# Performance work log

Hardware: AMD Instinct MI355X
Metric: run time of the kernel (lower is better)

The kernel has to match this reference:

```python
import jax, jax.numpy as jnp
import numpy as np

NF, NC, LENGTH, BATCH = 64, 16, 2048, 256
WEIGHT_BI, WEIGHT_L2 = 0.01, 0.01
BETA = 2.5     # temporal soft-min/max sharpness (TemporalOperator beta=2.5)
KAPPA = 10.0   # logical soft-min/max sharpness (avm approximation)
EPSN = 1e-12


def setup_inputs() -> dict:
    key = jax.random.key(0)
    ks = jax.random.split(key, 11)
    x = jax.random.normal(ks[0], (BATCH, LENGTH, 2), dtype=jnp.float32)
    t1 = jax.random.uniform(ks[1], (NF,), minval=0.0, maxval=float(LENGTH // 2), dtype=jnp.float32)
    t2 = jax.random.uniform(ks[2], (NF,), minval=float(LENGTH // 2), maxval=float(LENGTH), dtype=jnp.float32)
    a = jax.random.uniform(ks[3], (NF,), dtype=jnp.float32)
    b = jax.random.uniform(ks[4], (NF,), dtype=jnp.float32)
    p1 = jax.random.uniform(ks[5], (NC, NF), dtype=jnp.float32)
    p2 = jax.random.uniform(ks[6], (1, NC), dtype=jnp.float32)
    tvar_temporal = jax.random.uniform(ks[7], (NF,), dtype=jnp.float32)
    tvar_logical1 = jax.random.uniform(ks[8], (NC,), dtype=jnp.float32)
    tvar_logical2 = jax.random.uniform(ks[9], (1,), dtype=jnp.float32)
    eps = jnp.full((1,), 0.1, dtype=jnp.float32)
    return dict(x=x, t1=t1, t2=t2, a=a, b=b, p1=p1, p2=p2,
                tvar_temporal=tvar_temporal, tvar_logical1=tvar_logical1,
                tvar_logical2=tvar_logical2, eps=eps)


def _ste(v, v_new):
    # torch clamps parameter .data under no_grad -> value changes, grad is identity
    return v + jax.lax.stop_gradient(v_new - v)


def _wsel(r, logw, sharp):
    # weighted soft-max (sharp>0) / soft-min (sharp<0) along last axis
    s = jax.nn.softmax(sharp * r + logw, axis=-1)
    return jnp.sum(s * r, axis=-1)


def reference(x, t1, t2, a, b, p1, p2, tvar_temporal, tvar_logical1, tvar_logical2, eps):
    # --- in-place parameter maintenance (clamp under no_grad in torch) ---
    p1 = _ste(p1, jnp.clip(p1, 0.0, 1.0))
    p2 = _ste(p2, jnp.clip(p2, 0.0, 1.0))
    tvt = _ste(tvar_temporal, jnp.clip(tvar_temporal, 0.0, 1.0))
    tvl1 = _ste(tvar_logical1, jnp.clip(tvar_logical1, 0.0, 1.0))
    tvl2 = _ste(tvar_logical2, jnp.clip(tvar_logical2, 0.0, 1.0))
    t1c = jnp.clip(t1, 0.0, LENGTH - 1.0)
    t2c = jnp.clip(t2, 0.0, LENGTH - 1.0)
    t1c = jnp.where(t1c >= t2c - 1.0, t2c - 1.0, t1c)
    t1u = _ste(t1, t1c)
    t2u = _ste(t2, t2c)

    # --- predicates (vectorized over all nf features; dim = i % 2) ---
    dims = jnp.arange(NF) % 2
    rp = a[None, None, :] * x[:, :, dims] - b[None, None, :]     # [B, T, NF]
    rp = jnp.transpose(rp, (0, 2, 1))                             # [B, NF, T]

    # --- temporal operators: smooth window [t1, t2] + soft min/max over time ---
    tg = jnp.arange(LENGTH, dtype=x.dtype)
    w = jax.nn.sigmoid(BETA * (tg[None, :] - t1u[:, None])) * \
        jax.nn.sigmoid(BETA * (t2u[:, None] - tg[None, :]))       # [NF, T]
    logw = jnp.log(w + EPSN)[None]                                # [1, NF, T]
    rmax = _wsel(rp, logw, BETA)                                  # eventually  [B, NF]
    rmin = _wsel(rp, logw, -BETA)                                 # always      [B, NF]
    r1 = tvt[None, :] * rmax + (1.0 - tvt[None, :]) * rmin        # [B, NF]

    # --- logical layer 1: weighted soft OR/AND over features, per clause ---
    logp1 = jnp.log(p1 + EPSN)[None]                              # [1, NC, NF]
    r1e = r1[:, None, :]                                          # [B, NC, NF]
    r_or = _wsel(r1e, logp1, KAPPA)
    r_and = _wsel(r1e, logp1, -KAPPA)
    r2 = tvl1[None, :] * r_or + (1.0 - tvl1[None, :]) * r_and     # [B, NC]

    # --- logical layer 2: combine clauses ---
    logp2 = jnp.log(p2[0] + EPSN)[None]                           # [1, NC]
    r_or2 = _wsel(r2, logp2, KAPPA)
    r_and2 = _wsel(r2, logp2, -KAPPA)
    r = tvl2[0] * r_or2 + (1.0 - tvl2[0]) * r_and2                # [B]

    # --- regularizers ---
    bi = WEIGHT_BI * (jnp.sum(tvt * (1.0 - tvt)) + jnp.sum(tvl1 * (1.0 - tvl1)) +
                      jnp.sum(tvl2 * (1.0 - tvl2)) + jnp.sum(p1 * (1.0 - p1)) +
                      jnp.sum(p2 * (1.0 - p2)))
    l2 = WEIGHT_L2 * (jnp.sum(p1 * p1) + jnp.sum(p2 * p2))
    reg = bi + l2
    return r, reg
```

## Files before the change

### kernel.cpp

```cpp
#include <hip/hip_runtime.h>
#include <math.h>

#define NF 64
#define NC 16
#define LEN 2048
#define BATCH 256
#define BETA 2.5f
#define KAPPA 10.0f
#define EPSN 1e-12f
#define LOG2E 1.4426950408889634f

#define TPB 1024
#define NQ (TPB / NF)
#define CHUNK (LEN / NQ)

__device__ __forceinline__ float clip01(float v) { return fminf(fmaxf(v, 0.0f), 1.0f); }

__device__ __forceinline__ float fexp2(float x) {
#if __has_builtin(__builtin_amdgcn_exp2f)
    return __builtin_amdgcn_exp2f(x);
#else
    return exp2f(x);
#endif
}

__device__ __forceinline__ float frcp(float x) {
#if __has_builtin(__builtin_amdgcn_rcpf)
    return __builtin_amdgcn_rcpf(x);
#else
    return 1.0f / x;
#endif
}

__global__ __launch_bounds__(TPB) void fused_kernel(
    const float* __restrict__ x, const float* __restrict__ t1g,
    const float* __restrict__ t2g, const float* __restrict__ av,
    const float* __restrict__ bv, const float* __restrict__ p1,
    const float* __restrict__ p2, const float* __restrict__ tvt_,
    const float* __restrict__ tvl1_, const float* __restrict__ tvl2_,
    float* __restrict__ out) {
    __shared__ float4 redQ[NQ][NF];
    __shared__ float r1s[NF];
    __shared__ float r2s[NC];

    const int b = blockIdx.x;
    const int tid = threadIdx.x;
    const int f = tid & (NF - 1);
    const int q = tid >> 6;
    const int ch = f & 1;

    const float B2 = BETA * LOG2E;
    const float KL = KAPPA * LOG2E;

    const float a = av[f];
    const float A2 = B2 * a;

    float t1c = fminf(fmaxf(t1g[f], 0.0f), (float)(LEN - 1));
    float t2c = fminf(fmaxf(t2g[f], 0.0f), (float)(LEN - 1));
    t1c = fminf(t1c, t2c - 1.0f);
    const float c1 = B2 * t1c;
    const float c2 = -B2 * t2c;

    const int t0 = q * CHUNK;
    const float4* xp4 = (const float4*)(x + (size_t)b * (LEN * 2) + 2 * t0);

    float Sp0 = 0.f, Xp0 = 0.f, Sm0 = 0.f, Xm0 = 0.f;
    float Sp1 = 0.f, Xp1 = 0.f, Sm1 = 0.f, Xm1 = 0.f;
#pragma unroll 4
    for (int k2 = 0; k2 < CHUNK / 2; ++k2) {
        float4 v = xp4[k2];
        float xa = ch ? v.y : v.x;
        float xb = ch ? v.w : v.z;
        float tfa = (float)(t0 + 2 * k2);
        float tfb = tfa + 1.0f;

        {
            float g1 = fmaf(-B2, tfa, c1);
            float g2 = fmaf(B2, tfa, c2);
            float den = (1.0f + fexp2(g1)) * (1.0f + fexp2(g2));
            float w = frcp(den);
            float P = fexp2(A2 * xa);
            float Pm = frcp(P);
            float tp = P * w, tm = Pm * w;
            Sp0 += tp; Xp0 = fmaf(tp, xa, Xp0);
            Sm0 += tm; Xm0 = fmaf(tm, xa, Xm0);
        }
        {
            float g1 = fmaf(-B2, tfb, c1);
            float g2 = fmaf(B2, tfb, c2);
            float den = (1.0f + fexp2(g1)) * (1.0f + fexp2(g2));
            float w = frcp(den);
            float P = fexp2(A2 * xb);
            float Pm = frcp(P);
            float tp = P * w, tm = Pm * w;
            Sp1 += tp; Xp1 = fmaf(tp, xb, Xp1);
            Sm1 += tm; Xm1 = fmaf(tm, xb, Xm1);
        }
    }

    redQ[q][f] = make_float4(Sp0 + Sp1, Xp0 + Xp1, Sm0 + Sm1, Xm0 + Xm1);

    if (b == 0 && q == NQ - 1) {
        const int l = f;
        float acc = 0.0f;
#pragma unroll
        for (int i = 0; i < 16; ++i) {
            float p = clip01(p1[i * NF + l]);
            acc += 0.01f * (p * (1.0f - p)) + 0.01f * (p * p);
        }
        {
            float c = clip01(tvt_[l]);
            acc += 0.01f * (c * (1.0f - c));
        }
        if (l < NC) {
            float p = clip01(p2[l]);
            acc += 0.01f * (p * (1.0f - p)) + 0.01f * (p * p);
            float c = clip01(tvl1_[l]);
            acc += 0.01f * (c * (1.0f - c));
        }
        if (l == 0) {
            float c = clip01(tvl2_[0]);
            acc += 0.01f * (c * (1.0f - c));
        }
#pragma unroll
        for (int d = 1; d < 64; d <<= 1) acc += __shfl_xor(acc, d);
        if (l == 0) out[BATCH] = acc;
    }

    __syncthreads();
    if (tid >= 64) return;

    const int l = tid;
    float ax = 0.f, ay = 0.f, az = 0.f, aw = 0.f;
#pragma unroll
    for (int s = 0; s < NQ; ++s) {
        float4 v = redQ[s][l];
        ax += v.x; ay += v.y; az += v.z; aw += v.w;
    }
    {
        float af = av[l], bf = bv[l];
        float tvt = clip01(tvt_[l]);
        float rmax = af * (ay / ax);
        float rmin = af * (aw / az);
        r1s[l] = tvt * rmax + (1.0f - tvt) * rmin - bf;
    }

    {
        const int c = l & 15;
        const int j = l >> 4;
        float so = 0.f, wo = 0.f, sa = 0.f, wa = 0.f;
#pragma unroll
        for (int i = 0; i < 16; ++i) {
            int ff = j * 16 + i;
            float r1v = r1s[ff];
            float lg = __log2f(clip01(p1[c * NF + ff]) + EPSN);
            float z = KL * r1v;
            float eo = fexp2(z + lg);
            float ea = fexp2(lg - z);
            so += eo; wo = fmaf(eo, r1v, wo);
            sa += ea; wa = fmaf(ea, r1v, wa);
        }
#pragma unroll
        for (int d = 16; d < 64; d <<= 1) {
            so += __shfl_xor(so, d);
            wo += __shfl_xor(wo, d);
            sa += __shfl_xor(sa, d);
            wa += __shfl_xor(wa, d);
        }
        if (l < NC) {
            float tvl1 = clip01(tvl1_[l]);
            r2s[l] = tvl1 * (wo / so) + (1.0f - tvl1) * (wa / sa);
        }
    }

    if (l == 0) {
        float so = 0.f, wo = 0.f, sa = 0.f, wa = 0.f;
#pragma unroll
        for (int c = 0; c < NC; ++c) {
            float lg = __log2f(clip01(p2[c]) + EPSN);
            float r2v = r2s[c];
            float z = KL * r2v;
            float eo = fexp2(z + lg);
            float ea = fexp2(lg - z);
            so += eo; wo = fmaf(eo, r2v, wo);
            sa += ea; wa = fmaf(ea, r2v, wa);
        }
        float tvl2 = clip01(tvl2_[0]);
        out[b] = tvl2 * (wo / so) + (1.0f - tvl2) * (wa / sa);
    }
}

extern "C" void kernel_launch(void* const* d_in, const int* in_sizes, int n_in,
                              void* d_out, int out_size, void* d_ws, size_t ws_size,
                              hipStream_t stream) {
    const float* x    = (const float*)d_in[0];
    const float* t1   = (const float*)d_in[1];
    const float* t2   = (const float*)d_in[2];
    const float* a    = (const float*)d_in[3];
    const float* bv   = (const float*)d_in[4];
    const float* p1   = (const float*)d_in[5];
    const float* p2   = (const float*)d_in[6];
    const float* tvt  = (const float*)d_in[7];
    const float* tvl1 = (const float*)d_in[8];
    const float* tvl2 = (const float*)d_in[9];
    float* out = (float*)d_out;

    fused_kernel<<<BATCH, TPB, 0, stream>>>(x, t1, t2, a, bv, p1, p2,
                                            tvt, tvl1, tvl2, out);
}
```

Baseline: 26.90 us.

## Precompute batch-independent log temporal weights in a separate kernel

Adds a pre-pass kernel that computes the log2 of the sigmoid time-window weights for every feature and time step once, storing them in workspace in a float4-friendly layout, and also computes the regularizer. The main kernel then reads these weights and folds them into the exponent, replacing per-element window exps and reciprocals with two exp2 calls per element. This removes work that was repeated for each of the 256 batch rows. In exchange it adds a second launch and 512KB of extra workspace traffic, and it falls back to the old inline kernel if no workspace is available.

After: 26.05 us (median of 2 runs). 1.03x faster.

```diff
diff --git a/kernel.cpp b/kernel.cpp
--- a/kernel.cpp
+++ b/kernel.cpp
@@ -32,7 +32,178 @@
 #endif
 }
 
-__global__ __launch_bounds__(TPB) void fused_kernel(
+#define LW_BLOCKS ((NF * LEN / 4) / 256)
+
+__global__ __launch_bounds__(256) void lw_reg_kernel(
+    const float* __restrict__ t1, const float* __restrict__ t2,
+    const float* __restrict__ p1, const float* __restrict__ p2,
+    const float* __restrict__ tvt, const float* __restrict__ tvl1,
+    const float* __restrict__ tvl2, float4* __restrict__ lwT4,
+    float* __restrict__ out) {
+    const int bid = blockIdx.x;
+    const int tid = threadIdx.x;
+
+    if (bid == LW_BLOCKS) {
+        __shared__ float red[256];
+        float acc = 0.0f;
+        for (int i = tid; i < NC * NF; i += 256) {
+            float p = clip01(p1[i]);
+            acc += 0.01f * (p * (1.0f - p)) + 0.01f * (p * p);
+        }
+        if (tid < NC) {
+            float p = clip01(p2[tid]);
+            acc += 0.01f * (p * (1.0f - p)) + 0.01f * (p * p);
+        }
+        if (tid < NF) {
+            float c = clip01(tvt[tid]);
+            acc += 0.01f * (c * (1.0f - c));
+        }
+        if (tid < NC) {
+            float c = clip01(tvl1[tid]);
+            acc += 0.01f * (c * (1.0f - c));
+        }
+        if (tid == 0) {
+            float c = clip01(tvl2[0]);
+            acc += 0.01f * (c * (1.0f - c));
+        }
+        red[tid] = acc;
+        __syncthreads();
+        for (int s = 128; s > 0; s >>= 1) {
+            if (tid < s) red[tid] += red[tid + s];
+            __syncthreads();
+        }
+        if (tid == 0) out[BATCH] = red[0];
+        return;
+    }
+
+    int idx = bid * 256 + tid;
+    int f = idx & (NF - 1);
+    int g = idx >> 6;
+    float t1c = fminf(fmaxf(t1[f], 0.0f), (float)(LEN - 1));
+    float t2c = fminf(fmaxf(t2[f], 0.0f), (float)(LEN - 1));
+    t1c = fminf(t1c, t2c - 1.0f);
+    float4 r;
+#pragma unroll
+    for (int j = 0; j < 4; ++j) {
+        float t = (float)(4 * g + j);
+        float su = 1.0f / (1.0f + __expf(-BETA * (t - t1c)));
+        float sv = 1.0f / (1.0f + __expf(-BETA * (t2c - t)));
+        ((float*)&r)[j] = __log2f(su * sv + EPSN);
+    }
+    lwT4[idx] = r;
+}
+
+__global__ __launch_bounds__(TPB) void fused_main(
+    const float* __restrict__ x, const float4* __restrict__ lwT4,
+    const float* __restrict__ av, const float* __restrict__ bv,
+    const float* __restrict__ p1, const float* __restrict__ p2,
+    const float* __restrict__ tvt_, const float* __restrict__ tvl1_,
+    const float* __restrict__ tvl2_, float* __restrict__ out) {
+    __shared__ float4 redQ[NQ][NF];
+    __shared__ float r1s[NF];
+    __shared__ float r2s[NC];
+
+    const int b = blockIdx.x;
+    const int tid = threadIdx.x;
+    const int f = tid & (NF - 1);
+    const int q = tid >> 6;
+    const int ch = f & 1;
+
+    const float B2 = BETA * LOG2E;
+    const float KL = KAPPA * LOG2E;
+    const float A2 = B2 * av[f];
+
+    const int t0 = q * CHUNK;
+    const float4* lw4 = lwT4 + (t0 >> 2) * NF + f;
+    const float4* xp4 = (const float4*)(x + (size_t)b * (LEN * 2) + 2 * t0);
+
+    float Sp0 = 0.f, Xp0 = 0.f, Sm0 = 0.f, Xm0 = 0.f;
+    float Sp1 = 0.f, Xp1 = 0.f, Sm1 = 0.f, Xm1 = 0.f;
+#pragma unroll 4
+    for (int g = 0; g < CHUNK / 4; ++g) {
+        float4 lw = lw4[g * NF];
+        float4 u0 = xp4[2 * g];
+        float4 u1 = xp4[2 * g + 1];
+        float xa = ch ? u0.y : u0.x;
+        float xb = ch ? u0.w : u0.z;
+        float xc = ch ? u1.y : u1.x;
+        float xd = ch ? u1.w : u1.z;
+        float e;
+        e = fexp2(fmaf(A2, xa, lw.x));  Sp0 += e; Xp0 = fmaf(e, xa, Xp0);
+        e = fexp2(fmaf(-A2, xa, lw.x)); Sm0 += e; Xm0 = fmaf(e, xa, Xm0);
+        e = fexp2(fmaf(A2, xb, lw.y));  Sp1 += e; Xp1 = fmaf(e, xb, Xp1);
+        e = fexp2(fmaf(-A2, xb, lw.y)); Sm1 += e; Xm1 = fmaf(e, xb, Xm1);
+        e = fexp2(fmaf(A2, xc, lw.z));  Sp0 += e; Xp0 = fmaf(e, xc, Xp0);
+        e = fexp2(fmaf(-A2, xc, lw.z)); Sm0 += e; Xm0 = fmaf(e, xc, Xm0);
+        e = fexp2(fmaf(A2, xd, lw.w));  Sp1 += e; Xp1 = fmaf(e, xd, Xp1);
+        e = fexp2(fmaf(-A2, xd, lw.w)); Sm1 += e; Xm1 = fmaf(e, xd, Xm1);
+    }
+
+    redQ[q][f] = make_float4(Sp0 + Sp1, Xp0 + Xp1, Sm0 + Sm1, Xm0 + Xm1);
+    __syncthreads();
+    if (tid >= 64) return;
+
+    const int l = tid;
+    float ax = 0.f, ay = 0.f, az = 0.f, aw = 0.f;
+#pragma unroll
+    for (int s = 0; s < NQ; ++s) {
+        float4 v = redQ[s][l];
+        ax += v.x; ay += v.y; az += v.z; aw += v.w;
+    }
+    {
+        float af = av[l], bf = bv[l];
+        float tvt = clip01(tvt_[l]);
+        float rmax = af * (ay / ax);
+        float rmin = af * (aw / az);
+        r1s[l] = tvt * rmax + (1.0f - tvt) * rmin - bf;
+    }
+
+    {
+        const int c = l & 15;
+        const int j = l >> 4;
+        float so = 0.f, wo = 0.f, sa = 0.f, wa = 0.f;
+#pragma unroll
+        for (int i = 0; i < 16; ++i) {
+            int ff = j * 16 + i;
+            float r1v = r1s[ff];
+            float lg = __log2f(clip01(p1[c * NF + ff]) + EPSN);
+            float z = KL * r1v;
+            float eo = fexp2(z + lg);
+            float ea = fexp2(lg - z);
+            so += eo; wo = fmaf(eo, r1v, wo);
+            sa += ea; wa = fmaf(ea, r1v, wa);
+        }
+#pragma unroll
+        for (int d = 16; d < 64; d <<= 1) {
+            so += __shfl_xor(so, d);
+            wo += __shfl_xor(wo, d);
+            sa += __shfl_xor(sa, d);
+            wa += __shfl_xor(wa, d);
+        }
+        if (l < NC) {
+            float tvl1 = clip01(tvl1_[l]);
+            r2s[l] = tvl1 * (wo / so) + (1.0f - tvl1) * (wa / sa);
+        }
+    }
+
+    if (l == 0) {
+        float so = 0.f, wo = 0.f, sa = 0.f, wa = 0.f;
+#pragma unroll
+        for (int c = 0; c < NC; ++c) {
+            float lg = __log2f(clip01(p2[c]) + EPSN);
+            float r2v = r2s[c];
+            float z = KL * r2v;
+            float eo = fexp2(z + lg);
+            float ea = fexp2(lg - z);
+            so += eo; wo = fmaf(eo, r2v, wo);
+            sa += ea; wa = fmaf(ea, r2v, wa);
+        }
+        float tvl2 = clip01(tvl2_[0]);
+        out[b] = tvl2 * (wo / so) + (1.0f - tvl2) * (wa / sa);
+    }
+}
+
+__global__ __launch_bounds__(TPB) void fused_inline(
     const float* __restrict__ x, const float* __restrict__ t1g,
     const float* __restrict__ t2g, const float* __restrict__ av,
     const float* __restrict__ bv, const float* __restrict__ p1,
@@ -51,9 +222,7 @@
 
     const float B2 = BETA * LOG2E;
     const float KL = KAPPA * LOG2E;
-
-    const float a = av[f];
-    const float A2 = B2 * a;
+    const float A2 = B2 * av[f];
 
     float t1c = fminf(fmaxf(t1g[f], 0.0f), (float)(LEN - 1));
     float t2c = fminf(fmaxf(t2g[f], 0.0f), (float)(LEN - 1));
@@ -73,7 +242,6 @@
         float xb = ch ? v.w : v.z;
         float tfa = (float)(t0 + 2 * k2);
         float tfb = tfa + 1.0f;
-
         {
             float g1 = fmaf(-B2, tfa, c1);
             float g2 = fmaf(B2, tfa, c2);
@@ -144,7 +312,6 @@
         float rmin = af * (aw / az);
         r1s[l] = tvt * rmax + (1.0f - tvt) * rmin - bf;
     }
-
     {
         const int c = l & 15;
         const int j = l >> 4;
@@ -172,7 +339,6 @@
             r2s[l] = tvl1 * (wo / so) + (1.0f - tvl1) * (wa / sa);
         }
     }
-
     if (l == 0) {
         float so = 0.f, wo = 0.f, sa = 0.f, wa = 0.f;
 #pragma unroll
@@ -205,6 +371,16 @@
     const float* tvl2 = (const float*)d_in[9];
     float* out = (float*)d_out;
 
-    fused_kernel<<<BATCH, TPB, 0, stream>>>(x, t1, t2, a, bv, p1, p2,
-                                            tvt, tvl1, tvl2, out);
-}
+    const size_t lw_bytes = (size_t)(NF * LEN) * sizeof(float);
+
+    if (d_ws && ws_size >= lw_bytes) {
+        float4* lwT4 = (float4*)d_ws;
+        lw_reg_kernel<<<LW_BLOCKS + 1, 256, 0, stream>>>(t1, t2, p1, p2, tvt, tvl1,
+                                                         tvl2, lwT4, out);
+        fused_main<<<BATCH, TPB, 0, stream>>>(x, lwT4, a, bv, p1, p2,
+                                              tvt, tvl1, tvl2, out);
+    } else {
+        fused_inline<<<BATCH, TPB, 0, stream>>>(x, t1, t2, a, bv, p1, p2,
+                                                tvt, tvl1, tvl2, out);
+    }
+}
```
